# Kernel optimization log

Measured on AMD Instinct MI355X. Metric: run time of the kernel, lower is better.

Reference implementation:

```python
import jax, jax.numpy as jnp
import numpy as np

NUM_NODE = 50000
NUM_EDGE = 1_600_000
NUM_REL = 512
DIM = 64


def setup_inputs() -> dict:
    key = jax.random.key(0)
    k1, k2, k3, k4, k5, k6 = jax.random.split(key, 6)
    inp = jax.random.normal(k1, (NUM_NODE, DIM), dtype=jnp.float32)
    boundary = jax.random.normal(k2, (NUM_NODE, DIM), dtype=jnp.float32)
    node_in = jax.random.randint(k3, (NUM_EDGE,), 0, NUM_NODE)
    node_out = jax.random.randint(k4, (NUM_EDGE,), 0, NUM_NODE)
    rel = jax.random.randint(k5, (NUM_EDGE,), 0, NUM_REL)
    edge_list = jnp.stack([node_in, node_out, rel], axis=1).astype(jnp.int32)
    edge_weight = jnp.ones((NUM_EDGE,), dtype=jnp.float32)
    relation_weight = jax.random.normal(k6, (NUM_REL, DIM), dtype=jnp.float32)
    W = jax.random.normal(jax.random.fold_in(key, 7), (DIM, DIM), dtype=jnp.float32) / np.sqrt(DIM)
    b = jnp.zeros((DIM,), dtype=jnp.float32)
    return {"input": inp, "boundary": boundary, "edge_list": edge_list,
            "edge_weight": edge_weight, "relation_weight": relation_weight,
            "W": W, "b": b}


def reference(input, boundary, edge_list, edge_weight, relation_weight, W, b):
    node_in = edge_list[:, 0]
    node_out = edge_list[:, 1]
    rel = edge_list[:, 2]
    # message: DistMult = x_src * r_e   [E, D]
    msg = input[node_in] * relation_weight[rel]
    msg = msg * edge_weight[:, None]
    # std aggregation: sum and sq_sum scatters, boundary acts as an extra self-message
    s = jax.ops.segment_sum(msg, node_out, num_segments=NUM_NODE) + boundary
    sq = jax.ops.segment_sum(msg * msg, node_out, num_segments=NUM_NODE) + boundary * boundary
    deg = jax.ops.segment_sum(jnp.ones_like(edge_weight), node_out, num_segments=NUM_NODE)
    deg1 = (deg + 1.0)[:, None]  # degree_out + 1 (boundary counted)
    update = jnp.sqrt(jnp.clip(sq / deg1 - (s / deg1) ** 2, 1e-6))
    # add_model: single Linear (MLP with num_mlp_layer=1, no trailing activation)
    return update @ W.T + b
```

## Files before the change

### kernel.cpp

```cpp
#include <hip/hip_runtime.h>
#include <hip/hip_bf16.h>

#define NN  50000
#define NE  1600000
#define DIM 64
#define NBK 391

#define OFF_FLAGS  0
#define OFF_BCURP  8
#define OFF_EIDX   6272

#define CHUNK 4096
#define SBCAP 7936

typedef __bf16 bf16x8 __attribute__((ext_vector_type(8)));
typedef __bf16 bf16x4 __attribute__((ext_vector_type(4)));
typedef float  f32x4  __attribute__((ext_vector_type(4)));

__device__ __forceinline__ float loadF(const void* p, int i, int bf) {
  if (bf) return __bfloat162float(((const __hip_bfloat16*)p)[i]);
  return ((const float*)p)[i];
}

__device__ __forceinline__ float4 loadF4(const void* p, int i4, int bf) {
  if (bf) {
    ushort4 u = ((const ushort4*)p)[i4];
    float4 f;
    union { unsigned int ui; float fl; } c;
    c.ui = (unsigned int)u.x << 16; f.x = c.fl;
    c.ui = (unsigned int)u.y << 16; f.y = c.fl;
    c.ui = (unsigned int)u.z << 16; f.z = c.fl;
    c.ui = (unsigned int)u.w << 16; f.w = c.fl;
    return f;
  }
  return ((const float4*)p)[i4];
}

__device__ __forceinline__ void accumF(float4 a, float4 r,
                                       float4& s4, float4& q4) {
  float tx = a.x * r.x, ty = a.y * r.y, tz = a.z * r.z, tw = a.w * r.w;
  s4.x += tx; q4.x = fmaf(tx, tx, q4.x);
  s4.y += ty; q4.y = fmaf(ty, ty, q4.y);
  s4.z += tz; q4.z = fmaf(tz, tz, q4.z);
  s4.w += tw; q4.w = fmaf(tw, tw, q4.w);
}

__global__ void k_detect(const void* input, const void* boundary,
                         const void* relw, const void* W, const void* ew,
                         int* flags, int* bcurp) {
  __shared__ int cnt;
  int t = threadIdx.x;
  const void* arrs[4] = {input, boundary, relw, W};
  for (int a = 0; a < 4; ++a) {
    if (t == 0) cnt = 0;
    __syncthreads();
    const unsigned short* u = (const unsigned short*)arrs[a];
    unsigned ex = (u[2 * t] >> 7) & 0xFF;
    if (ex >= 100 && ex <= 140) atomicAdd(&cnt, 1);
    __syncthreads();
    if (t == 0) flags[a] = (cnt >= 32) ? 1 : 0;
    __syncthreads();
  }
  if (t == 0) {
    flags[4] = (((const unsigned short*)ew)[0] == 0x3F80) ? 1 : 0;
    flags[5] = 1;
  }
  for (int i = t; i < NBK * 16; i += 64) bcurp[i] = 0;
}

__global__ __launch_bounds__(256) void k_ew(const void* __restrict__ ew,
                                            int* __restrict__ flags) {
  int bfE = flags[4];
  int c0 = blockIdx.x * 8192;
  int bad = 0;
  for (int i = threadIdx.x; i < 8192; i += 256) {
    int e = c0 + i;
    if (e < NE && loadF(ew, e, bfE) != 1.0f) bad = 1;
  }
  if (bad) flags[5] = 0;
}

__global__ __launch_bounds__(1024) void k_parta(
    const int* __restrict__ el, int* __restrict__ bcurp,
    int* __restrict__ eidx, const int* __restrict__ flags,
    int gb0, int gb1, int padcap) {
  __shared__ int stage[CHUNK];
  __shared__ unsigned short sbk[CHUNK];
  __shared__ int lh[NBK], lbase[NBK], lh2[NBK], gbs[NBK];
  __shared__ int sc[256];
  __shared__ int total;
  int t = threadIdx.x;
  int nb = gb1 - gb0;
  int c0 = blockIdx.x * CHUNK;
  int ones = flags[5];
  for (int i = t; i < nb; i += 1024) { lh[i] = 0; lh2[i] = 0; }
  __syncthreads();

  int rec[4], bb[4];
  #pragma unroll
  for (int j = 0; j < 4; ++j) {
    int e = c0 + j * 1024 + t;
    bb[j] = -1; rec[j] = 0;
    if (e < NE) {
      int n0 = el[e * 3], n1 = el[e * 3 + 1], n2 = el[e * 3 + 2];
      int b = (n1 >> 7) - gb0;
      if (b >= 0 && b < nb) {
        bb[j] = b;
        rec[j] = ones ? (n0 | (n2 << 16) | ((n1 & 127) << 25))
                      : (e | ((n1 & 127) << 25));
        atomicAdd(&lh[b], 1);
      }
    }
  }
  __syncthreads();

  int a0 = 0, a1 = 0;
  if (t < 256) {
    a0 = (2 * t < nb) ? lh[2 * t] : 0;
    a1 = (2 * t + 1 < nb) ? lh[2 * t + 1] : 0;
    sc[t] = a0 + a1;
  }
  __syncthreads();
  for (int off = 1; off < 256; off <<= 1) {
    int v = 0;
    if (t < 256 && t >= off) v = sc[t - off];
    __syncthreads();
    if (t < 256) sc[t] += v;
    __syncthreads();
  }
  if (t < 256) {
    int excl = sc[t] - (a0 + a1);
    if (2 * t < nb) {
      lbase[2 * t] = excl;
      if (a0 > 0) gbs[2 * t] = atomicAdd(&bcurp[(gb0 + 2 * t) * 16], a0);
    }
    if (2 * t + 1 < nb) {
      lbase[2 * t + 1] = excl + a0;
      if (a1 > 0)
        gbs[2 * t + 1] = atomicAdd(&bcurp[(gb0 + 2 * t + 1) * 16], a1);
    }
    if (t == 255) total = sc[255];
  }
  __syncthreads();

  #pragma unroll
  for (int j = 0; j < 4; ++j) {
    if (bb[j] >= 0) {
      int r = atomicAdd(&lh2[bb[j]], 1);
      int slot = lbase[bb[j]] + r;
      stage[slot] = rec[j];
      sbk[slot] = (unsigned short)bb[j];
    }
  }
  __syncthreads();

  int tot = total;
  for (int i = t; i < tot; i += 1024) {
    int b = sbk[i];
    int slot = gbs[b] + (i - lbase[b]);
    if (slot < padcap) eidx[(long)b * padcap + slot] = stage[i];
  }
}

__global__ __launch_bounds__(1024, 8) void k_node(
    const void* __restrict__ input, const void* __restrict__ boundary,
    const int* __restrict__ el, const void* __restrict__ ew,
    const void* __restrict__ relw, const void* __restrict__ W,
    const void* __restrict__ bv, const int* __restrict__ bcurp,
    const int* __restrict__ eidx, const int* __restrict__ flags,
    void* __restrict__ out, int gb0, int hi, int padcap) {
  __shared__ int ld[SBCAP];
  __shared__ int ld2[SBCAP];
  __shared__ int lstart[128], lend[128], lcnt[128];
  __bf16 (*updb)[72] = reinterpret_cast<__bf16(*)[72]>(ld);

  int bfI = flags[0], bfB = flags[1], bfR = flags[2], bfW = flags[3],
      bfE = flags[4], ones = flags[5];
  int t = threadIdx.x;
  int wv = t >> 6, ln = t & 63;
  int g = ln >> 4;
  int k = ln & 15;
  int q = ln >> 4;
  int B = gb0 + blockIdx.x;
  int n0 = B * 128;
  int cnt = bcurp[B * 16];
  int fast = (cnt <= SBCAP) && (cnt <= padcap);
  const int* myeidx = eidx + (long)blockIdx.x * padcap;

  if (t < 128) lcnt[t] = 0;
  __syncthreads();
  if (fast) {
    for (int i = t; i < cnt; i += 1024) ld[i] = myeidx[i];
    __syncthreads();
    for (int i = t; i < cnt; i += 1024)
      atomicAdd(&lcnt[(((unsigned)ld[i]) >> 25) & 127], 1);
  }
  __syncthreads();
  if (t < 128) lend[t] = lcnt[t];
  __syncthreads();
  for (int off = 1; off < 128; off <<= 1) {
    int v = 0;
    if (t < 128 && t >= off) v = lend[t - off];
    __syncthreads();
    if (t < 128) lend[t] += v;
    __syncthreads();
  }
  if (t < 128) { lstart[t] = lend[t] - lcnt[t]; lcnt[t] = 0; }
  __syncthreads();
  if (fast) {
    for (int i = t; i < cnt; i += 1024) {
      int rec = ld[i];
      int l = (((unsigned)rec) >> 25) & 127;
      int r = atomicAdd(&lcnt[l], 1);
      ld2[lstart[l] + r] = rec;
    }
  }
  __syncthreads();

  const float4* inp4 = (const float4*)input;
  const float4* rw4  = (const float4*)relw;
  int hot = (!bfI && !bfR && ones) ? 1 : 0;

  for (int rr = 0; rr < 8; ++rr) {
    int row = wv * 8 + rr;
    int n = n0 + row;
    if (n >= hi) {
      if (g == 0) *(bf16x4*)&updb[row][4 * k] =
          bf16x4{(__bf16)0.f, (__bf16)0.f, (__bf16)0.f, (__bf16)0.f};
      continue;
    }
    float4 s4 = {0.f,0.f,0.f,0.f}, q4 = {0.f,0.f,0.f,0.f};
    float degf = 0.f;
    if (fast) {
      int start = lstart[row], end = lend[row];
      degf = (float)(end - start);
      if (hot) {
        for (int base = start; base < end; base += 64) {
          int mm = end - base; if (mm > 64) mm = 64;
          int rec = 0;
          if (ln < mm) rec = ld2[base + ln];
          int jq = mm >> 2;
          int jmax = (mm + 3) >> 2;
          int j = 0;
          for (; j + 4 <= jq; j += 4) {
            int pk0 = __shfl(rec, j * 4 + g);
            int pk1 = __shfl(rec, j * 4 + 4 + g);
            int pk2 = __shfl(rec, j * 4 + 8 + g);
            int pk3 = __shfl(rec, j * 4 + 12 + g);
            float4 a0 = inp4[(pk0 & 0xFFFF) * 16 + k];
            float4 r0 = rw4[((pk0 >> 16) & 0x1FF) * 16 + k];
            float4 a1 = inp4[(pk1 & 0xFFFF) * 16 + k];
            float4 r1 = rw4[((pk1 >> 16) & 0x1FF) * 16 + k];
            float4 a2 = inp4[(pk2 & 0xFFFF) * 16 + k];
            float4 r2 = rw4[((pk2 >> 16) & 0x1FF) * 16 + k];
            float4 a3 = inp4[(pk3 & 0xFFFF) * 16 + k];
            float4 r3 = rw4[((pk3 >> 16) & 0x1FF) * 16 + k];
            accumF(a0, r0, s4, q4);
            accumF(a1, r1, s4, q4);
            accumF(a2, r2, s4, q4);
            accumF(a3, r3, s4, q4);
          }
          for (; j < jq; ++j) {
            int pk = __shfl(rec, j * 4 + g);
            float4 a = inp4[(pk & 0xFFFF) * 16 + k];
            float4 r = rw4[((pk >> 16) & 0x1FF) * 16 + k];
            accumF(a, r, s4, q4);
          }
          for (; j < jmax; ++j) {
            int slot = j * 4 + g;
            int pk = __shfl(rec, slot & 63);
            float wsel = (slot < mm) ? 1.0f : 0.0f;
            float4 a = inp4[(pk & 0xFFFF) * 16 + k];
            float4 r = rw4[((pk >> 16) & 0x1FF) * 16 + k];
            float tx = a.x*r.x, ty = a.y*r.y, tz = a.z*r.z, tw = a.w*r.w;
            s4.x = fmaf(wsel, tx, s4.x); q4.x = fmaf(wsel*tx, tx, q4.x);
            s4.y = fmaf(wsel, ty, s4.y); q4.y = fmaf(wsel*ty, ty, q4.y);
            s4.z = fmaf(wsel, tz, s4.z); q4.z = fmaf(wsel*tz, tz, q4.z);
            s4.w = fmaf(wsel, tw, s4.w); q4.w = fmaf(wsel*tw, tw, q4.w);
          }
        }
      } else {
        for (int base = start; base < end; base += 64) {
          int mm = end - base; if (mm > 64) mm = 64;
          int rec = 0; float wrec = 0.0f;
          if (ln < mm) {
            rec = ld2[base + ln] & 0x1FFFFFF;
            if (!ones) wrec = loadF(ew, rec, bfE);
          }
          int jmax = (mm + 3) >> 2;
          for (int j = 0; j < jmax; ++j) {
            int slot = j * 4 + g;
            int rj = __shfl(rec, slot);
            int nin, rl; float wj;
            if (ones) { nin = rj & 0xFFFF; rl = (rj >> 16) & 0x1FF; wj = 1.0f; }
            else      { nin = el[rj * 3]; rl = el[rj * 3 + 2];
                        wj = __shfl(wrec, slot); }
            float wsel = (slot < mm) ? wj : 0.0f;
            float4 a = loadF4(input, nin * 16 + k, bfI);
            float4 r = loadF4(relw, rl * 16 + k, bfR);
            float tx = a.x*r.x, ty = a.y*r.y, tz = a.z*r.z, tw = a.w*r.w;
            s4.x = fmaf(wsel, tx, s4.x); q4.x = fmaf(wsel*tx, tx, q4.x);
            s4.y = fmaf(wsel, ty, s4.y); q4.y = fmaf(wsel*ty, ty, q4.y);
            s4.z = fmaf(wsel, tz, s4.z); q4.z = fmaf(wsel*tz, tz, q4.z);
            s4.w = fmaf(wsel, tw, s4.w); q4.w = fmaf(wsel*tw, tw, q4.w);
          }
        }
      }
    } else {
      float degc = 0.f;
      for (int e0 = g; e0 < NE; e0 += 4) {
        int nout = el[e0 * 3 + 1];
        if (nout != n) continue;
        degc += 1.0f;
        int nin = el[e0 * 3], rl = el[e0 * 3 + 2];
        float wj = ones ? 1.0f : loadF(ew, e0, bfE);
        float4 a = loadF4(input, nin * 16 + k, bfI);
        float4 r = loadF4(relw, rl * 16 + k, bfR);
        float tx = wj*a.x*r.x, ty = wj*a.y*r.y, tz = wj*a.z*r.z,
              tw = wj*a.w*r.w;
        s4.x += tx; q4.x = fmaf(tx, tx, q4.x);
        s4.y += ty; q4.y = fmaf(ty, ty, q4.y);
        s4.z += tz; q4.z = fmaf(tz, tz, q4.z);
        s4.w += tw; q4.w = fmaf(tw, tw, q4.w);
      }
      degc += __shfl_xor(degc, 16); degc += __shfl_xor(degc, 32);
      degf = degc;
    }
    s4.x += __shfl_xor(s4.x, 16); s4.x += __shfl_xor(s4.x, 32);
    s4.y += __shfl_xor(s4.y, 16); s4.y += __shfl_xor(s4.y, 32);
    s4.z += __shfl_xor(s4.z, 16); s4.z += __shfl_xor(s4.z, 32);
    s4.w += __shfl_xor(s4.w, 16); s4.w += __shfl_xor(s4.w, 32);
    q4.x += __shfl_xor(q4.x, 16); q4.x += __shfl_xor(q4.x, 32);
    q4.y += __shfl_xor(q4.y, 16); q4.y += __shfl_xor(q4.y, 32);
    q4.z += __shfl_xor(q4.z, 16); q4.z += __shfl_xor(q4.z, 32);
    q4.w += __shfl_xor(q4.w, 16); q4.w += __shfl_xor(q4.w, 32);
    if (g == 0) {
      float4 b4 = loadF4(boundary, n * 16 + k, bfB);
      float dg = degf + 1.0f;
      float sv, qv;
      bf16x4 u;
      sv = (s4.x + b4.x) / dg; qv = (q4.x + b4.x * b4.x) / dg;
      u[0] = (__bf16)sqrtf(fmaxf(qv - sv * sv, 1e-6f));
      sv = (s4.y + b4.y) / dg; qv = (q4.y + b4.y * b4.y) / dg;
      u[1] = (__bf16)sqrtf(fmaxf(qv - sv * sv, 1e-6f));
      sv = (s4.z + b4.z) / dg; qv = (q4.z + b4.z * b4.z) / dg;
      u[2] = (__bf16)sqrtf(fmaxf(qv - sv * sv, 1e-6f));
      sv = (s4.w + b4.w) / dg; qv = (q4.w + b4.w * b4.w) / dg;
      u[3] = (__bf16)sqrtf(fmaxf(qv - sv * sv, 1e-6f));
      *(bf16x4*)&updb[row][4 * k] = u;
    }
  }
  __syncthreads();

  int tt = wv >> 1, chh = wv & 1;
  bf16x8 af0 = *(const bf16x8*)&updb[tt * 16 + (ln & 15)][q * 8];
  bf16x8 af1 = *(const bf16x8*)&updb[tt * 16 + (ln & 15)][32 + q * 8];
  #pragma unroll
  for (int hh = 0; hh < 2; ++hh) {
    int cc = chh * 32 + hh * 16 + (ln & 15);
    bf16x8 bfr0, bfr1;
    #pragma unroll
    for (int j = 0; j < 8; ++j) {
      bfr0[j] = (__bf16)loadF(W, cc * 64 + q * 8 + j, bfW);
      bfr1[j] = (__bf16)loadF(W, cc * 64 + 32 + q * 8 + j, bfW);
    }
    float bias = loadF(bv, cc, bfW);
    f32x4 accv = {0.f, 0.f, 0.f, 0.f};
    accv = __builtin_amdgcn_mfma_f32_16x16x32_bf16(af0, bfr0, accv, 0, 0, 0);
    accv = __builtin_amdgcn_mfma_f32_16x16x32_bf16(af1, bfr1, accv, 0, 0, 0);
    #pragma unroll
    for (int i = 0; i < 4; ++i) {
      int nn = n0 + tt * 16 + q * 4 + i;
      if (nn < hi) {
        float v = accv[i] + bias;
        if (bfI) ((__hip_bfloat16*)out)[nn * 64 + cc] = __float2bfloat16(v);
        else     ((float*)out)[nn * 64 + cc] = v;
      }
    }
  }
}

extern "C" void kernel_launch(void* const* d_in, const int* in_sizes, int n_in,
                              void* d_out, int out_size, void* d_ws, size_t ws_size,
                              hipStream_t stream) {
  const void* input    = d_in[0];
  const void* boundary = d_in[1];
  const int*  edges    = (const int*)d_in[2];
  const void* eweight  = d_in[3];
  const void* relw     = d_in[4];
  const void* W        = d_in[5];
  const void* bv       = d_in[6];

  int* wsI    = (int*)d_ws;
  int* flags  = wsI + OFF_FLAGS;
  int* bcurp  = wsI + OFF_BCURP;
  int* eidx   = wsI + OFF_EIDX;

  long avail = (long)(ws_size / 4) - OFF_EIDX;
  if (avail < 1) avail = 1;
  int padcap = 8192;
  long bfit = avail / padcap;
  if (bfit < 1) { padcap = (int)avail; bfit = 1; }
  if (bfit > NBK) bfit = NBK;
  int npass = (int)((NBK + bfit - 1) / bfit);

  k_detect<<<1, 64, 0, stream>>>(input, boundary, relw, W, eweight,
                                 flags, bcurp);
  k_ew<<<(NE + 8191) / 8192, 256, 0, stream>>>(eweight, flags);

  const int PA_NB = (NE + CHUNK - 1) / CHUNK;
  for (int p = 0; p < npass; ++p) {
    int gb0 = (int)((long)NBK * p / npass);
    int gb1 = (int)((long)NBK * (p + 1) / npass);
    int hi = (gb1 * 128 < NN) ? gb1 * 128 : NN;
    k_parta<<<PA_NB, 1024, 0, stream>>>(edges, bcurp, eidx, flags,
                                        gb0, gb1, padcap);
    k_node<<<gb1 - gb0, 1024, 0, stream>>>(
        input, boundary, edges, eweight, relw, W, bv, bcurp, eidx, flags,
        d_out, gb0, hi, padcap);
  }
}
```

Baseline: 213.8 us.

## Split node kernel into quarter-bucket blocks and double partition chunk size

```diff
diff --git a/kernel.cpp b/kernel.cpp
--- a/kernel.cpp
+++ b/kernel.cpp
@@ -10,8 +10,8 @@
 #define OFF_BCURP  8
 #define OFF_EIDX   6272
 
-#define CHUNK 4096
-#define SBCAP 7936
+#define CHUNK 8192
+#define QCAP  2304
 
 typedef __bf16 bf16x8 __attribute__((ext_vector_type(8)));
 typedef __bf16 bf16x4 __attribute__((ext_vector_type(4)));
@@ -96,9 +96,9 @@
   for (int i = t; i < nb; i += 1024) { lh[i] = 0; lh2[i] = 0; }
   __syncthreads();
 
-  int rec[4], bb[4];
+  int rec[8], bb[8];
   #pragma unroll
-  for (int j = 0; j < 4; ++j) {
+  for (int j = 0; j < 8; ++j) {
     int e = c0 + j * 1024 + t;
     bb[j] = -1; rec[j] = 0;
     if (e < NE) {
@@ -144,7 +144,7 @@
   __syncthreads();
 
   #pragma unroll
-  for (int j = 0; j < 4; ++j) {
+  for (int j = 0; j < 8; ++j) {
     if (bb[j] >= 0) {
       int r = atomicAdd(&lh2[bb[j]], 1);
       int slot = lbase[bb[j]] + r;
@@ -162,16 +162,17 @@
   }
 }
 
-__global__ __launch_bounds__(1024, 8) void k_node(
+__global__ __launch_bounds__(256, 8) void k_node(
     const void* __restrict__ input, const void* __restrict__ boundary,
     const int* __restrict__ el, const void* __restrict__ ew,
     const void* __restrict__ relw, const void* __restrict__ W,
     const void* __restrict__ bv, const int* __restrict__ bcurp,
     const int* __restrict__ eidx, const int* __restrict__ flags,
     void* __restrict__ out, int gb0, int hi, int padcap) {
-  __shared__ int ld[SBCAP];
-  __shared__ int ld2[SBCAP];
-  __shared__ int lstart[128], lend[128], lcnt[128];
+  __shared__ int ld[QCAP];
+  __shared__ int ld2[QCAP];
+  __shared__ int lstart[32], lend[32], lcnt[32];
+  __shared__ int nf, ovf;
   __bf16 (*updb)[72] = reinterpret_cast<__bf16(*)[72]>(ld);
 
   int bfI = flags[0], bfB = flags[1], bfR = flags[2], bfW = flags[3],
@@ -181,38 +182,51 @@
   int g = ln >> 4;
   int k = ln & 15;
   int q = ln >> 4;
-  int B = gb0 + blockIdx.x;
-  int n0 = B * 128;
+  int Bl = blockIdx.x >> 2;
+  int B  = gb0 + Bl;
+  int quarter = blockIdx.x & 3;
+  int n0 = B * 128 + quarter * 32;
   int cnt = bcurp[B * 16];
-  int fast = (cnt <= SBCAP) && (cnt <= padcap);
-  const int* myeidx = eidx + (long)blockIdx.x * padcap;
-
-  if (t < 128) lcnt[t] = 0;
-  __syncthreads();
+  const int* myeidx = eidx + (long)Bl * padcap;
+
+  if (t == 0) { nf = 0; ovf = (cnt > padcap) ? 1 : 0; }
+  if (t < 32) lcnt[t] = 0;
+  __syncthreads();
+
+  int cl = cnt < padcap ? cnt : padcap;
+  for (int i = t; i < cl; i += 256) {
+    int rc = myeidx[i];
+    if ((((unsigned)rc) >> 30) == (unsigned)quarter) {
+      int p = atomicAdd(&nf, 1);
+      if (p < QCAP) ld[p] = rc; else ovf = 1;
+    }
+  }
+  __syncthreads();
+  int fast = !ovf;
+  int nq = nf < QCAP ? nf : QCAP;
+
   if (fast) {
-    for (int i = t; i < cnt; i += 1024) ld[i] = myeidx[i];
-    __syncthreads();
-    for (int i = t; i < cnt; i += 1024)
-      atomicAdd(&lcnt[(((unsigned)ld[i]) >> 25) & 127], 1);
-  }
-  __syncthreads();
-  if (t < 128) lend[t] = lcnt[t];
-  __syncthreads();
-  for (int off = 1; off < 128; off <<= 1) {
+    for (int i = t; i < nq; i += 256)
+      atomicAdd(&lcnt[(((unsigned)ld[i]) >> 25) & 31], 1);
+  }
+  __syncthreads();
+  if (t < 32) lend[t] = lcnt[t];
+  __syncthreads();
+  for (int off = 1; off < 32; off <<= 1) {
     int v = 0;
-    if (t < 128 && t >= off) v = lend[t - off];
-    __syncthreads();
-    if (t < 128) lend[t] += v;
-    __syncthreads();
-  }
-  if (t < 128) { lstart[t] = lend[t] - lcnt[t]; lcnt[t] = 0; }
+    if (t < 32 && t >= off) v = lend[t - off];
+    __syncthreads();
+    if (t < 32) lend[t] += v;
+    __syncthreads();
+  }
+  if (t < 32) { lstart[t] = lend[t] - lcnt[t]; lcnt[t] = 0; }
   __syncthreads();
   if (fast) {
-    for (int i = t; i < cnt; i += 1024) {
-      int rec = ld[i];
-      int l = (((unsigned)rec) >> 25) & 127;
+    for (int i = t; i < nq; i += 256) {
+      int rc = ld[i];
+      int l = (((unsigned)rc) >> 25) & 31;
       int r = atomicAdd(&lcnt[l], 1);
-      ld2[lstart[l] + r] = rec;
+      ld2[lstart[l] + r] = rc;
     }
   }
   __syncthreads();
@@ -415,7 +429,7 @@
     int hi = (gb1 * 128 < NN) ? gb1 * 128 : NN;
     k_parta<<<PA_NB, 1024, 0, stream>>>(edges, bcurp, eidx, flags,
                                         gb0, gb1, padcap);
-    k_node<<<gb1 - gb0, 1024, 0, stream>>>(
+    k_node<<<(gb1 - gb0) * 4, 256, 0, stream>>>(
         input, boundary, edges, eweight, relw, W, bv, bcurp, eidx, flags,
         d_out, gb0, hi, padcap);
   }
```

Result: no change. 212.5 us (-0.6%).
